# Kernel optimization log

Measured on AMD Instinct MI355X. Metric: run time of the kernel, lower is better.

## Reference

```python
import jax, jax.numpy as jnp
import numpy as np

B, T, D, H = 8, 2048, 1024, 128  # batch, seq, input_size, head_size


def setup_inputs() -> dict:
    key = jax.random.key(0)
    kx, kq, kk, kv = jax.random.split(key, 4)
    s = 1.0 / np.sqrt(D)
    return {
        "x": jax.random.normal(kx, (B, T, D), dtype=jnp.float32),
        "Wq": jax.random.normal(kq, (D, H), dtype=jnp.float32) * s,
        "Wk": jax.random.normal(kk, (D, H), dtype=jnp.float32) * s,
        "Wv": jax.random.normal(kv, (D, H), dtype=jnp.float32) * s,
    }


def reference(x, Wq, Wk, Wv):
    # projections (Linear, no bias)
    q = jnp.einsum("btd,dh->bth", x, Wq)
    k = jnp.einsum("btd,dh->bth", x, Wk)
    v = jnp.einsum("btd,dh->bth", x, Wv)
    scale = H ** (-0.5)
    scores = jnp.einsum("bth,bsh->bts", q, k) * scale  # [B,T,T]
    t = x.shape[1]
    causal = jnp.tril(jnp.ones((t, t), dtype=bool))
    scores = jnp.where(causal, scores, -jnp.inf)
    attn = jax.nn.softmax(scores, axis=-1)  # dropout p=0.0 -> identity
    out = jnp.einsum("bts,bsh->bth", attn, v)
    return out
```

## Files before the change

### kernel.cpp

```cpp
#include <hip/hip_runtime.h>
#include <math.h>

#define B_ 8
#define T_ 2048
#define D_ 1024
#define H_ 128
#define BT (B_ * T_)

typedef short bf16x8 __attribute__((ext_vector_type(8)));
typedef float f32x4 __attribute__((ext_vector_type(4)));

static constexpr float SCALE = 0.08838834764831845f;

__device__ inline unsigned short f2b(float f) {
  unsigned int u = __float_as_uint(f);
  u += 0x7FFF + ((u >> 16) & 1);
  return (unsigned short)(u >> 16);
}
__device__ inline unsigned int pk2(float a, float b) {
  return (unsigned int)f2b(a) | ((unsigned int)f2b(b) << 16);
}

__device__ __forceinline__ void gll16(const void* g, void* l) {
  __builtin_amdgcn_global_load_lds(
      (const __attribute__((address_space(1))) void*)g,
      (__attribute__((address_space(3))) void*)l, 16, 0, 0);
}

__global__ __launch_bounds__(256) void wcvt_kernel(
    const float* __restrict__ Wq, const float* __restrict__ Wk,
    const float* __restrict__ Wv, short* __restrict__ Wt) {
  const int sel = blockIdx.y;
  const float* W = sel == 0 ? Wq : (sel == 1 ? Wk : Wv);
  short* dst = Wt + (size_t)sel * D_ * H_;
  int slot = blockIdx.x * 256 + threadIdx.x;
  int d = slot >> 5, hg = slot & 31;
  float4 w = *(const float4*)(W + (size_t)d * H_ + hg * 4);
  dst[(size_t)(hg * 4 + 0) * D_ + d] = (short)f2b(w.x);
  dst[(size_t)(hg * 4 + 1) * D_ + d] = (short)f2b(w.y);
  dst[(size_t)(hg * 4 + 2) * D_ + d] = (short)f2b(w.z);
  dst[(size_t)(hg * 4 + 3) * D_ + d] = (short)f2b(w.w);
}

__global__ __launch_bounds__(256) void proj_kernel(
    const float* __restrict__ x, const short* __restrict__ Wt,
    short* __restrict__ qb, short* __restrict__ kb, short* __restrict__ vtb) {
  __shared__ alignas(16) char smem[36864];
  short* Xs = (short*)smem;
  short* Ws = (short*)(smem + 16384);

  const int tid = threadIdx.x;
  const int wave = tid >> 6, lane = tid & 63;
  const int ln = lane & 15, quad = lane >> 4;
  const int mw = wave & 1, nw = wave >> 1;
  const int sel = blockIdx.y;
  const int row0 = blockIdx.x * 128;
  const short* W = Wt + (size_t)sel * (size_t)(D_ * H_);

  f32x4 acc[4][4];
#pragma unroll
  for (int mi = 0; mi < 4; ++mi)
#pragma unroll
    for (int ni = 0; ni < 4; ++ni) acc[mi][ni] = (f32x4){0.f, 0.f, 0.f, 0.f};

  for (int s = 0; s < 16; ++s) {
    const int k0 = s * 64;
    if (s) __syncthreads();

#pragma unroll
    for (int j = 0; j < 4; ++j) {
      const int rbase = wave * 32 + j * 8;
      const int n = rbase + (lane >> 3);
      const int gp = (lane & 7) ^ (n & 7);
      gll16(W + (size_t)n * D_ + k0 + gp * 8, (char*)Ws + rbase * 128);
    }

    {
      float4 xr[8];
#pragma unroll
      for (int i = 0; i < 8; ++i) {
        int fid = tid + i * 256;
        int r = fid >> 4, g4 = fid & 15;
        xr[i] = *(const float4*)(x + (size_t)(row0 + r) * D_ + k0 + g4 * 4);
      }
#pragma unroll
      for (int i = 0; i < 8; ++i) {
        int fid = tid + i * 256;
        int r = fid >> 4, g4 = fid & 15;
        int g = g4 >> 1, half = g4 & 1;
        unsigned int* p = (unsigned int*)&Xs[r * 64 + ((g ^ (r & 7)) * 8) + half * 4];
        p[0] = pk2(xr[i].x, xr[i].y);
        p[1] = pk2(xr[i].z, xr[i].w);
      }
    }
    __syncthreads();

#pragma unroll
    for (int kk = 0; kk < 2; ++kk) {
      bf16x8 a[4];
#pragma unroll
      for (int mi = 0; mi < 4; ++mi) {
        int r = mw * 64 + mi * 16 + ln;
        int g = kk * 4 + quad;
        a[mi] = *(bf16x8*)&Xs[r * 64 + ((g ^ (r & 7)) * 8)];
      }
#pragma unroll
      for (int ni = 0; ni < 4; ++ni) {
        int n = nw * 64 + ni * 16 + ln;
        int g = kk * 4 + quad;
        bf16x8 bb = *(bf16x8*)&Ws[n * 64 + ((g ^ (n & 7)) * 8)];
#pragma unroll
        for (int mi = 0; mi < 4; ++mi)
          acc[mi][ni] = __builtin_amdgcn_mfma_f32_16x16x32_bf16(a[mi], bb, acc[mi][ni], 0, 0, 0);
      }
    }
  }

  __syncthreads();
  short* Cs = (short*)smem;
  if (sel < 2) {
    short* out = sel ? kb : qb;
#pragma unroll
    for (int mi = 0; mi < 4; ++mi)
#pragma unroll
      for (int ni = 0; ni < 4; ++ni)
#pragma unroll
        for (int rr = 0; rr < 4; ++rr)
          Cs[(mw * 64 + mi * 16 + quad * 4 + rr) * 136 + nw * 64 + ni * 16 + ln] =
              (short)f2b(acc[mi][ni][rr]);
    __syncthreads();
#pragma unroll
    for (int i = 0; i < 8; ++i) {
      int slot = tid + i * 256;
      int r = slot >> 4, g = slot & 15;
      *(int4*)(out + (size_t)(row0 + r) * H_ + g * 8) = *(int4*)&Cs[r * 136 + g * 8];
    }
  } else {
#pragma unroll
    for (int mi = 0; mi < 4; ++mi)
#pragma unroll
      for (int ni = 0; ni < 4; ++ni)
#pragma unroll
        for (int rr = 0; rr < 4; ++rr)
          Cs[(nw * 64 + ni * 16 + ln) * 136 + mw * 64 + mi * 16 + quad * 4 + rr] =
              (short)f2b(acc[mi][ni][rr]);
    __syncthreads();
    const int b = row0 >> 11, t0 = row0 & 2047;
#pragma unroll
    for (int i = 0; i < 8; ++i) {
      int slot = tid + i * 256;
      int h = slot >> 4, g = slot & 15;
      *(int4*)(vtb + (size_t)(b * H_ + h) * T_ + t0 + g * 8) = *(int4*)&Cs[h * 136 + g * 8];
    }
  }
}

__global__ __launch_bounds__(256) void attn_kernel(
    const short* __restrict__ qb, const short* __restrict__ kb,
    const short* __restrict__ vtb, float* __restrict__ out) {
  __shared__ alignas(16) short Ks[64 * 136];
  __shared__ alignas(16) short Vt[128 * 72];
  __shared__ alignas(16) float Sf[32 * 65];
  __shared__ alignas(16) short P[32 * 72];
  __shared__ float aA[32], lL[32];

  const int tid = threadIdx.x;
  const int wave = tid >> 6, lane = tid & 63;
  const int ln = lane & 15, quad = lane >> 4;
  const int b = blockIdx.x >> 6;
  const int tile = 63 - (blockIdx.x & 63);
  const int q0 = tile * 32;

  bf16x8 qfr[2][4];
#pragma unroll
  for (int m = 0; m < 2; ++m)
#pragma unroll
    for (int kk = 0; kk < 4; ++kk)
      qfr[m][kk] = *(const bf16x8*)(qb + (size_t)(b * T_ + q0 + m * 16 + ln) * H_ +
                                    kk * 32 + quad * 8);

  f32x4 oacc[2][2];
#pragma unroll
  for (int m = 0; m < 2; ++m)
#pragma unroll
    for (int nt = 0; nt < 2; ++nt) oacc[m][nt] = (f32x4){0.f, 0.f, 0.f, 0.f};

  const int srow = tid >> 3, l8 = tid & 7;
  float m_run = -INFINITY, l_run = 0.f;

  const int nch = ((q0 + 31) >> 6) + 1;
  for (int ch = 0; ch < nch; ++ch) {
    const int s0 = ch * 64;
    if (ch) __syncthreads();
#pragma unroll
    for (int w = 0; w < 4; ++w) {
      int i = tid + w * 256;
      int r = i >> 4, g = i & 15;
      *(int4*)&Ks[r * 136 + g * 8] =
          *(const int4*)(kb + (size_t)(b * T_ + s0 + r) * H_ + g * 8);
      int h = i >> 3, g2 = i & 7;
      *(int4*)&Vt[h * 72 + g2 * 8] =
          *(const int4*)(vtb + (size_t)(b * H_ + h) * T_ + s0 + g2 * 8);
    }
    __syncthreads();

    f32x4 sacc[2];
    sacc[0] = (f32x4){0.f, 0.f, 0.f, 0.f};
    sacc[1] = (f32x4){0.f, 0.f, 0.f, 0.f};
#pragma unroll
    for (int kk = 0; kk < 4; ++kk) {
      bf16x8 bk = *(bf16x8*)&Ks[(wave * 16 + ln) * 136 + kk * 32 + quad * 8];
#pragma unroll
      for (int m = 0; m < 2; ++m)
        sacc[m] = __builtin_amdgcn_mfma_f32_16x16x32_bf16(qfr[m][kk], bk, sacc[m], 0, 0, 0);
    }
#pragma unroll
    for (int m = 0; m < 2; ++m)
#pragma unroll
      for (int r = 0; r < 4; ++r)
        Sf[(m * 16 + quad * 4 + r) * 65 + wave * 16 + ln] = sacc[m][r];
    __syncthreads();

    float sv[8];
    const int qg = q0 + srow;
#pragma unroll
    for (int i = 0; i < 8; ++i) {
      float s = Sf[srow * 65 + l8 * 8 + i] * SCALE;
      sv[i] = (s0 + l8 * 8 + i <= qg) ? s : -INFINITY;
    }
    float mx = sv[0];
#pragma unroll
    for (int i = 1; i < 8; ++i) mx = fmaxf(mx, sv[i]);
    mx = fmaxf(mx, __shfl_xor(mx, 1));
    mx = fmaxf(mx, __shfl_xor(mx, 2));
    mx = fmaxf(mx, __shfl_xor(mx, 4));
    const float mnew = fmaxf(m_run, mx);
    const float alpha = __expf(m_run - mnew);
    float p[8], ps = 0.f;
#pragma unroll
    for (int i = 0; i < 8; ++i) {
      p[i] = __expf(sv[i] - mnew);
      ps += p[i];
    }
    ps += __shfl_xor(ps, 1);
    ps += __shfl_xor(ps, 2);
    ps += __shfl_xor(ps, 4);
    l_run = l_run * alpha + ps;
    m_run = mnew;
    int4 pw;
    pw.x = (int)pk2(p[0], p[1]);
    pw.y = (int)pk2(p[2], p[3]);
    pw.z = (int)pk2(p[4], p[5]);
    pw.w = (int)pk2(p[6], p[7]);
    *(int4*)&P[srow * 72 + l8 * 8] = pw;
    if (l8 == 0) aA[srow] = alpha;
    __syncthreads();

    const int h0 = wave * 32;
    float ar[2][4];
#pragma unroll
    for (int m = 0; m < 2; ++m)
#pragma unroll
      for (int r = 0; r < 4; ++r) ar[m][r] = aA[m * 16 + quad * 4 + r];
#pragma unroll
    for (int m = 0; m < 2; ++m)
#pragma unroll
      for (int nt = 0; nt < 2; ++nt)
#pragma unroll
        for (int r = 0; r < 4; ++r) oacc[m][nt][r] *= ar[m][r];
#pragma unroll
    for (int ks = 0; ks < 2; ++ks) {
      bf16x8 pa[2];
      pa[0] = *(bf16x8*)&P[ln * 72 + ks * 32 + quad * 8];
      pa[1] = *(bf16x8*)&P[(16 + ln) * 72 + ks * 32 + quad * 8];
#pragma unroll
      for (int nt = 0; nt < 2; ++nt) {
        bf16x8 bv = *(bf16x8*)&Vt[(h0 + nt * 16 + ln) * 72 + ks * 32 + quad * 8];
#pragma unroll
        for (int m = 0; m < 2; ++m)
          oacc[m][nt] = __builtin_amdgcn_mfma_f32_16x16x32_bf16(pa[m], bv, oacc[m][nt], 0, 0, 0);
      }
    }
  }

  if (l8 == 0) lL[srow] = l_run;
  __syncthreads();
  const int h0 = wave * 32;
#pragma unroll
  for (int m = 0; m < 2; ++m) {
    float linv[4];
#pragma unroll
    for (int r = 0; r < 4; ++r) linv[r] = 1.f / lL[m * 16 + quad * 4 + r];
#pragma unroll
    for (int nt = 0; nt < 2; ++nt)
#pragma unroll
      for (int r = 0; r < 4; ++r) {
        int row = q0 + m * 16 + quad * 4 + r;
        out[(size_t)(b * T_ + row) * H_ + h0 + nt * 16 + ln] = oacc[m][nt][r] * linv[r];
      }
  }
}

extern "C" void kernel_launch(void* const* d_in, const int* in_sizes, int n_in,
                              void* d_out, int out_size, void* d_ws, size_t ws_size,
                              hipStream_t stream) {
  const float* x  = (const float*)d_in[0];
  const float* Wq = (const float*)d_in[1];
  const float* Wk = (const float*)d_in[2];
  const float* Wv = (const float*)d_in[3];
  float* out = (float*)d_out;

  char* ws = (char*)d_ws;
  short* qb  = (short*)(ws);
  short* kb  = (short*)(ws + 4194304);
  short* vtb = (short*)(ws + 8388608);
  short* Wt  = (short*)(ws + 12582912);

  wcvt_kernel<<<dim3(128, 3), 256, 0, stream>>>(Wq, Wk, Wv, Wt);
  proj_kernel<<<dim3(BT / 128, 3), 256, 0, stream>>>(x, Wt, qb, kb, vtb);
  attn_kernel<<<dim3(8 * 64), 256, 0, stream>>>(qb, kb, vtb, out);
}
```

Before: 184.3 us.

## Double-buffer attention K/V tiles via async global-to-LDS loads and coalesce weight transpose

The attention kernel now double-buffers its K and V^T tiles in LDS. It issues direct global-to-LDS loads for the next chunk while computing the current one, and uses XOR-swizzled layouts in place of padded rows. The intent is to hide global load latency behind the MFMA and softmax work. The weight conversion kernel now transposes through shared memory, so its global writes become coalesced 16-byte stores instead of scattered 2-byte ones. The cost is double the LDS footprint for the K/V buffers, which may lower occupancy.

```diff
diff --git a/kernel.cpp b/kernel.cpp
--- a/kernel.cpp
+++ b/kernel.cpp
@@ -30,16 +30,29 @@
 __global__ __launch_bounds__(256) void wcvt_kernel(
     const float* __restrict__ Wq, const float* __restrict__ Wk,
     const float* __restrict__ Wv, short* __restrict__ Wt) {
+  __shared__ short Wls[128 * 72];
   const int sel = blockIdx.y;
   const float* W = sel == 0 ? Wq : (sel == 1 ? Wk : Wv);
+  const int d0 = blockIdx.x * 64;
+  const int tid = threadIdx.x;
+#pragma unroll
+  for (int i = 0; i < 8; ++i) {
+    int slot = tid + i * 256;
+    int r = slot >> 5, hg = slot & 31;
+    float4 w = *(const float4*)(W + (size_t)(d0 + r) * H_ + hg * 4);
+    Wls[(hg * 4 + 0) * 72 + r] = (short)f2b(w.x);
+    Wls[(hg * 4 + 1) * 72 + r] = (short)f2b(w.y);
+    Wls[(hg * 4 + 2) * 72 + r] = (short)f2b(w.z);
+    Wls[(hg * 4 + 3) * 72 + r] = (short)f2b(w.w);
+  }
+  __syncthreads();
   short* dst = Wt + (size_t)sel * D_ * H_;
-  int slot = blockIdx.x * 256 + threadIdx.x;
-  int d = slot >> 5, hg = slot & 31;
-  float4 w = *(const float4*)(W + (size_t)d * H_ + hg * 4);
-  dst[(size_t)(hg * 4 + 0) * D_ + d] = (short)f2b(w.x);
-  dst[(size_t)(hg * 4 + 1) * D_ + d] = (short)f2b(w.y);
-  dst[(size_t)(hg * 4 + 2) * D_ + d] = (short)f2b(w.z);
-  dst[(size_t)(hg * 4 + 3) * D_ + d] = (short)f2b(w.w);
+#pragma unroll
+  for (int i = 0; i < 4; ++i) {
+    int slot = tid + i * 256;
+    int h = slot >> 3, g = slot & 7;
+    *(int4*)(dst + (size_t)h * D_ + d0 + g * 8) = *(int4*)&Wls[h * 72 + g * 8];
+  }
 }
 
 __global__ __launch_bounds__(256) void proj_kernel(
@@ -74,7 +87,6 @@
       const int gp = (lane & 7) ^ (n & 7);
       gll16(W + (size_t)n * D_ + k0 + gp * 8, (char*)Ws + rbase * 128);
     }
-
     {
       float4 xr[8];
 #pragma unroll
@@ -158,8 +170,8 @@
 __global__ __launch_bounds__(256) void attn_kernel(
     const short* __restrict__ qb, const short* __restrict__ kb,
     const short* __restrict__ vtb, float* __restrict__ out) {
-  __shared__ alignas(16) short Ks[64 * 136];
-  __shared__ alignas(16) short Vt[128 * 72];
+  __shared__ alignas(16) short Ks[2][64 * 128];
+  __shared__ alignas(16) short Vt[2][128 * 64];
   __shared__ alignas(16) float Sf[32 * 65];
   __shared__ alignas(16) short P[32 * 72];
   __shared__ float aA[32], lL[32];
@@ -188,28 +200,41 @@
   const int srow = tid >> 3, l8 = tid & 7;
   float m_run = -INFINITY, l_run = 0.f;
 
+  auto stage = [&](int bf, int s0) {
+#pragma unroll
+    for (int j = 0; j < 4; ++j) {
+      const int rb = wave * 16 + j * 4;
+      const int r = rb + (lane >> 4);
+      const int gp = (lane & 15) ^ (r & 7);
+      gll16(kb + (size_t)(b * T_ + s0 + r) * H_ + gp * 8,
+            (char*)&Ks[bf][0] + rb * 256);
+    }
+#pragma unroll
+    for (int j = 0; j < 4; ++j) {
+      const int hb = wave * 32 + j * 8;
+      const int h = hb + (lane >> 3);
+      const int gp = (lane & 7) ^ (h & 7);
+      gll16(vtb + (size_t)(b * H_ + h) * T_ + s0 + gp * 8,
+            (char*)&Vt[bf][0] + hb * 128);
+    }
+  };
+
   const int nch = ((q0 + 31) >> 6) + 1;
+  stage(0, 0);
+
   for (int ch = 0; ch < nch; ++ch) {
+    const int cur = ch & 1;
     const int s0 = ch * 64;
-    if (ch) __syncthreads();
-#pragma unroll
-    for (int w = 0; w < 4; ++w) {
-      int i = tid + w * 256;
-      int r = i >> 4, g = i & 15;
-      *(int4*)&Ks[r * 136 + g * 8] =
-          *(const int4*)(kb + (size_t)(b * T_ + s0 + r) * H_ + g * 8);
-      int h = i >> 3, g2 = i & 7;
-      *(int4*)&Vt[h * 72 + g2 * 8] =
-          *(const int4*)(vtb + (size_t)(b * H_ + h) * T_ + s0 + g2 * 8);
-    }
-    __syncthreads();
+    __syncthreads();
+    if (ch + 1 < nch) stage(cur ^ 1, s0 + 64);
 
     f32x4 sacc[2];
     sacc[0] = (f32x4){0.f, 0.f, 0.f, 0.f};
     sacc[1] = (f32x4){0.f, 0.f, 0.f, 0.f};
 #pragma unroll
     for (int kk = 0; kk < 4; ++kk) {
-      bf16x8 bk = *(bf16x8*)&Ks[(wave * 16 + ln) * 136 + kk * 32 + quad * 8];
+      const int r = wave * 16 + ln;
+      bf16x8 bk = *(bf16x8*)&Ks[cur][r * 128 + (((kk * 4 + quad) ^ (r & 7)) * 8)];
 #pragma unroll
       for (int m = 0; m < 2; ++m)
         sacc[m] = __builtin_amdgcn_mfma_f32_16x16x32_bf16(qfr[m][kk], bk, sacc[m], 0, 0, 0);
@@ -275,7 +300,8 @@
       pa[1] = *(bf16x8*)&P[(16 + ln) * 72 + ks * 32 + quad * 8];
 #pragma unroll
       for (int nt = 0; nt < 2; ++nt) {
-        bf16x8 bv = *(bf16x8*)&Vt[(h0 + nt * 16 + ln) * 72 + ks * 32 + quad * 8];
+        const int n = h0 + nt * 16 + ln;
+        bf16x8 bv = *(bf16x8*)&Vt[cur][n * 64 + (((ks * 4 + quad) ^ (n & 7)) * 8)];
 #pragma unroll
         for (int m = 0; m < 2; ++m)
           oacc[m][nt] = __builtin_amdgcn_mfma_f32_16x16x32_bf16(pa[m], bv, oacc[m][nt], 0, 0, 0);
@@ -316,7 +342,7 @@
   short* vtb = (short*)(ws + 8388608);
   short* Wt  = (short*)(ws + 12582912);
 
-  wcvt_kernel<<<dim3(128, 3), 256, 0, stream>>>(Wq, Wk, Wv, Wt);
+  wcvt_kernel<<<dim3(D_ / 64, 3), 256, 0, stream>>>(Wq, Wk, Wv, Wt);
   proj_kernel<<<dim3(BT / 128, 3), 256, 0, stream>>>(x, Wt, qb, kb, vtb);
   attn_kernel<<<dim3(8 * 64), 256, 0, stream>>>(qb, kb, vtb, out);
 }
```

Measured after the change: 182.6 us. About the same (-0.9%).
